# Kernel tuning notes

Hardware: AMD Instinct MI355X
Metric: run time of the kernel (lower is better)

Reference implementation:

```python
import jax, jax.numpy as jnp
import numpy as np

N = 16384      # nodes
E = 262144     # edges (avg degree 16)
H = 128        # hidden_channels
F = 128        # num_filters
G = 50         # num_gaussians
L = 6          # num_interactions
NG = 16        # graphs in batch
CUTOFF = 10.0
BOX = 5.0
LN2 = 0.6931471805599453


def _ssp(x):  # ShiftedSoftplus
    return jax.nn.softplus(x) - LN2


def setup_inputs() -> dict:
    key = jax.random.key(0)
    ks = jax.random.split(key, 20)
    w = lambda k, shape: jax.random.normal(k, shape, dtype=jnp.float32) * 0.1
    return {
        "z": jax.random.randint(ks[0], (N,), 0, 2),
        "pos": jax.random.uniform(ks[1], (N, 3), dtype=jnp.float32) * BOX,
        "edge_index": jax.random.randint(ks[2], (2, E), 0, N),
        "batch": jnp.sort(jax.random.randint(ks[3], (N,), 0, NG)),
        "emb": w(ks[4], (2, H)),
        "mlp_w1": w(ks[5], (L, G, F)),
        "mlp_b1": jnp.zeros((L, F), jnp.float32),
        "mlp_w2": w(ks[6], (L, F, F)),
        "mlp_b2": jnp.zeros((L, F), jnp.float32),
        "cf_w1": w(ks[7], (L, H, F)),
        "cf_w2": w(ks[8], (L, F, H)),
        "cf_b2": jnp.zeros((L, H), jnp.float32),
        "lin_w": w(ks[9], (L, H, H)),
        "lin_b": jnp.zeros((L, H), jnp.float32),
        "out_w1": w(ks[10], (H, H // 2)),
        "out_b1": jnp.zeros((H // 2,), jnp.float32),
        "out_w2": w(ks[11], (H // 2, 1)),
        "out_b2": jnp.zeros((1,), jnp.float32),
    }


def reference(z, pos, edge_index, batch, emb, mlp_w1, mlp_b1, mlp_w2, mlp_b2,
              cf_w1, cf_w2, cf_b2, lin_w, lin_b, out_w1, out_b1, out_w2, out_b2):
    row, col = edge_index[0], edge_index[1]  # message flows row -> col
    dx = pos[row] - pos[col]
    dx = dx - jnp.round(dx / BOX) * BOX      # minimum-image PBC
    ew = jnp.sqrt(jnp.sum(dx * dx, axis=-1))               # [E]
    offset = jnp.linspace(0.0, CUTOFF, G)
    coeff = -0.5 / (offset[1] - offset[0]) ** 2
    ea = jnp.exp(coeff * (ew[:, None] - offset[None, :]) ** 2)  # [E, G]
    C = 0.5 * (jnp.cos(ew * jnp.pi / CUTOFF) + 1.0)
    C = C * (ew < CUTOFF).astype(C.dtype)                   # [E]

    h = emb[z]                                              # [N, H]
    for l in range(L):
        # continuous filter from smeared distances, with cosine cutoff
        W = (_ssp(ea @ mlp_w1[l] + mlp_b1[l]) @ mlp_w2[l] + mlp_b2[l]) * C[:, None]  # [E, F]
        xh = h @ cf_w1[l]                                   # [N, F] (lin1, no bias)
        msg = xh[row] * W                                   # gather x_j, modulate
        agg = jax.ops.segment_sum(msg, col, num_segments=N)  # scatter-add
        xc = agg @ cf_w2[l] + cf_b2[l]                      # [N, H] (lin2)
        h = h + (_ssp(xc) @ lin_w[l] + lin_b[l])            # residual interaction

    h = _ssp(h @ out_w1 + out_b1) @ out_w2 + out_b2         # [N, 1]
    out = jax.ops.segment_sum(h, batch, num_segments=NG)    # readout 'add'
    return jax.nn.sigmoid(out)                              # [NG, 1]
```

## Files before the change

### kernel.cpp

```cpp
#include <hip/hip_runtime.h>
#include <math.h>

#define N_NODES 16384
#define N_EDGES 262144
#define HDIM    128
#define NG50    50
#define NLAYER  6
#define NGRAPH  16
#define TROWS   1025
#define RMAXF   4.34f
#define WPL     16384

__device__ __forceinline__ float ssp_f(float x){
  return (x > 20.0f ? x : log1pf(__expf(x))) - 0.6931471805599453f;
}
__device__ __forceinline__ void fma4(float4& c, float a, const float4 b){
  c.x = fmaf(a,b.x,c.x); c.y = fmaf(a,b.y,c.y); c.z = fmaf(a,b.z,c.z); c.w = fmaf(a,b.w,c.w);
}
__device__ __forceinline__ unsigned short f2bf(float x){
  unsigned u = __float_as_uint(x);
  u += 0x7FFF + ((u>>16)&1);
  return (unsigned short)(u>>16);
}
__device__ __forceinline__ float bf2f(unsigned short u){
  return __uint_as_float(((unsigned)u)<<16);
}
__device__ __forceinline__ void load_chunk(float* Bs, const float* W, int kc, int tid){
  const float4* src = (const float4*)(W + kc*HDIM);
  float4* dst = (float4*)Bs;
  #pragma unroll
  for (int i=0;i<4;++i) dst[tid + i*256] = src[tid + i*256];
}

typedef __attribute__((ext_vector_type(8))) short bf16x8;
typedef __attribute__((ext_vector_type(4))) float f32x4;
__device__ __forceinline__ int swzf(int lin){ return lin ^ (((lin>>9)&7)<<4); }

__device__ __forceinline__ void split8(const float4 v0, const float4 v1, bf16x8& hi, bf16x8& lo){
  float x[8] = {v0.x,v0.y,v0.z,v0.w,v1.x,v1.y,v1.z,v1.w};
  #pragma unroll
  for (int i=0;i<8;++i){
    unsigned short h = f2bf(x[i]);
    hi[i] = (short)h;
    lo[i] = (short)f2bf(x[i] - bf2f(h));
  }
}

__global__ __launch_bounds__(256) void k_init_h(const int* __restrict__ z,
    const float* __restrict__ emb, float* __restrict__ h){
  int t = blockIdx.x*256 + threadIdx.x;
  int n = t >> 5, q = t & 31;
  ((float4*)h)[t] = ((const float4*)emb)[(z[n]<<5) + q];
}

#define TAB_R  4
#define TAB_NB 257
__global__ __launch_bounds__(256) void k_tab(const float* __restrict__ w1, const float* __restrict__ b1,
      const float* __restrict__ w2, const float* __restrict__ b2, float* __restrict__ tab){
  __shared__ float ea[TAB_R][52];
  __shared__ float sT[TAB_R][HDIM];
  __shared__ float part[2][TAB_R][HDIM];
  int l  = blockIdx.x / TAB_NB;
  int i0 = (blockIdx.x % TAB_NB) * TAB_R;
  int tid = threadIdx.x;
  int j    = tid & 127;
  int half = tid >> 7;
  const float* w1l = w1 + (size_t)l*NG50*HDIM;
  const float* w2l = w2 + (size_t)l*HDIM*HDIM;
  float* tabl = tab + (size_t)l*TROWS*HDIM;
  const float STEP = RMAXF/1024.0f;
  const float GS   = 10.0f/49.0f;
  const float GC   = -0.5f/(GS*GS);
  if (tid < TAB_R*NG50){
    int rr = tid / NG50, k = tid - rr*NG50;
    int ri = i0 + rr; if (ri > TROWS-1) ri = TROWS-1;
    float d = ri*STEP - k*GS;
    ea[rr][k] = __expf(GC*d*d);
  }
  __syncthreads();
  {
    float acc[TAB_R] = {0,0,0,0};
    int kb = half*25;
    for (int k=0;k<25;++k){
      float wv = w1l[(kb+k)*HDIM + j];
      #pragma unroll
      for (int r=0;r<TAB_R;++r) acc[r] = fmaf(ea[r][kb+k], wv, acc[r]);
    }
    #pragma unroll
    for (int r=0;r<TAB_R;++r) part[half][r][j] = acc[r];
  }
  __syncthreads();
  {
    float b1v = b1[(size_t)l*HDIM + j];
    #pragma unroll
    for (int rr=0;rr<2;++rr){
      int r = half*2 + rr;
      sT[r][j] = ssp_f(part[0][r][j] + part[1][r][j] + b1v);
    }
  }
  __syncthreads();
  {
    float o[TAB_R] = {0,0,0,0};
    int kb = half*64;
    #pragma unroll 4
    for (int k=0;k<64;++k){
      float wv = w2l[(kb+k)*HDIM + j];
      #pragma unroll
      for (int r=0;r<TAB_R;++r) o[r] = fmaf(sT[r][kb+k], wv, o[r]);
    }
    #pragma unroll
    for (int r=0;r<TAB_R;++r) part[half][r][j] = o[r];
  }
  __syncthreads();
  {
    float b2v = b2[(size_t)l*HDIM + j];
    #pragma unroll
    for (int rr=0;rr<2;++rr){
      int r = half*2 + rr;
      int ri = i0 + r;
      if (ri < TROWS){
        float rv = ri*STEP;
        float C = 0.5f*(cosf(rv*0.31415926535897931f) + 1.0f);
        tabl[(size_t)ri*HDIM + j] = (part[0][r][j] + part[1][r][j] + b2v)*C;
      }
    }
  }
}

__global__ __launch_bounds__(256) void k_pack(const float* __restrict__ tab, ushort4* __restrict__ tabp){
  size_t t = (size_t)blockIdx.x*256 + threadIdx.x;
  int lane = (int)(t & 63);
  size_t row = t >> 6;
  size_t l = row >> 10, i = row & 1023;
  const float* a = tab + (l*TROWS + i)*HDIM + lane*2;
  float2 av = *(const float2*)a;
  float2 bv = *(const float2*)(a + HDIM);
  ushort4 p;
  p.x = f2bf(av.x); p.y = f2bf(av.y); p.z = f2bf(bv.x); p.w = f2bf(bv.y);
  tabp[t] = p;
}

__global__ __launch_bounds__(256) void k_wpack(const float* __restrict__ cf_w2,
    const float* __restrict__ lin_w, const float* __restrict__ cf_w1, ushort* __restrict__ wp){
  int b   = blockIdx.x;
  int mat = b >> 3;
  int s   = (b & 7)*256 + threadIdx.x;
  const float* M = (mat < 6)  ? cf_w2 + (size_t)mat*HDIM*HDIM
                 : (mat < 12) ? lin_w + (size_t)(mat-6)*HDIM*HDIM
                              : cf_w1 + (size_t)(mat-12)*HDIM*HDIM;
  int ct = s >> 8, ks = (s >> 6) & 3, l = s & 63;
  int col = ct*16 + (l & 15);
  int r0  = ks*32 + (l >> 4)*8;
  ushort oh[8], ol[8];
  #pragma unroll
  for (int i=0;i<8;++i){
    float w = M[(size_t)(r0+i)*HDIM + col];
    oh[i] = f2bf(w);
    ol[i] = f2bf(w - bf2f(oh[i]));
  }
  ushort* dh = wp + (size_t)(2*mat)*WPL + (size_t)s*8;
  ushort* dl = dh + WPL;
  *(ushort4*)(dh+0) = make_ushort4(oh[0],oh[1],oh[2],oh[3]);
  *(ushort4*)(dh+4) = make_ushort4(oh[4],oh[5],oh[6],oh[7]);
  *(ushort4*)(dl+0) = make_ushort4(ol[0],ol[1],ol[2],ol[3]);
  *(ushort4*)(dl+4) = make_ushort4(ol[4],ol[5],ol[6],ol[7]);
}

__global__ __launch_bounds__(256) void k_hist(const int* __restrict__ ei, int* __restrict__ cursor){
  int e = blockIdx.x*256 + threadIdx.x;
  if (e < N_EDGES) atomicAdd(&cursor[ei[N_EDGES + e]], 1);
}
__global__ __launch_bounds__(1024) void k_scan(int* __restrict__ cursor, int* __restrict__ rowptr){
  __shared__ int sbuf[1024];
  int t = threadIdx.x;
  int base = t*16;
  int d[16]; int s = 0;
  #pragma unroll
  for (int i=0;i<16;++i){ d[i] = cursor[base+i]; s += d[i]; }
  sbuf[t] = s; __syncthreads();
  for (int off=1; off<1024; off<<=1){
    int v = sbuf[t];
    int add = (t >= off) ? sbuf[t-off] : 0;
    __syncthreads();
    sbuf[t] = v + add;
    __syncthreads();
  }
  int run = (t==0) ? 0 : sbuf[t-1];
  #pragma unroll
  for (int i=0;i<16;++i){ rowptr[base+i] = run; cursor[base+i] = run; run += d[i]; }
  if (t==1023) rowptr[N_NODES] = run;
}
__global__ __launch_bounds__(256) void k_fill(const int* __restrict__ ei, const float* __restrict__ pos,
    int* __restrict__ cursor, int* __restrict__ srcl, float* __restrict__ tl){
  int e = blockIdx.x*256 + threadIdx.x;
  if (e < N_EDGES){
    int a = ei[e];
    int c = ei[N_EDGES + e];
    float dx = pos[3*a+0] - pos[3*c+0];
    float dy = pos[3*a+1] - pos[3*c+1];
    float dz = pos[3*a+2] - pos[3*c+2];
    dx -= rintf(dx*0.2f)*5.0f;
    dy -= rintf(dy*0.2f)*5.0f;
    dz -= rintf(dz*0.2f)*5.0f;
    float r = sqrtf(fmaf(dx,dx,fmaf(dy,dy,dz*dz)));
    int slot = atomicAdd(&cursor[c], 1);
    srcl[slot] = a;
    tl[slot]   = r * (1024.0f/RMAXF);
  }
}

#define FR 16
__global__ __launch_bounds__(256,4) void k_gemm_xh(const float* __restrict__ A,
    const float* __restrict__ B, ushort4* __restrict__ Cb){
  __shared__ float Bs[32*HDIM];
  int tid = threadIdx.x;
  int m0 = blockIdx.x*FR;
  int tc = tid & 31, tr = tid >> 5;
  int j0 = tc*4;
  int lr0 = tr*2, lr1 = tr*2+1;
  float4 acc0 = make_float4(0,0,0,0), acc1 = acc0;
  const float* A0 = A + (size_t)(m0 + lr0)*HDIM;
  const float* A1 = A + (size_t)(m0 + lr1)*HDIM;
  for (int kc=0; kc<HDIM; kc+=32){
    __syncthreads();
    load_chunk(Bs, B, kc, tid);
    __syncthreads();
    #pragma unroll
    for (int kk=0; kk<32; kk+=4){
      float4 b0 = *(const float4*)(Bs + (kk+0)*HDIM + j0);
      float4 b1 = *(const float4*)(Bs + (kk+1)*HDIM + j0);
      float4 b2 = *(const float4*)(Bs + (kk+2)*HDIM + j0);
      float4 b3 = *(const float4*)(Bs + (kk+3)*HDIM + j0);
      float4 a0 = *(const float4*)(A0 + kc + kk);
      float4 a1 = *(const float4*)(A1 + kc + kk);
      fma4(acc0,a0.x,b0); fma4(acc0,a0.y,b1); fma4(acc0,a0.z,b2); fma4(acc0,a0.w,b3);
      fma4(acc1,a1.x,b0); fma4(acc1,a1.y,b1); fma4(acc1,a1.z,b2); fma4(acc1,a1.w,b3);
    }
  }
  ushort4 o;
  o.x=f2bf(acc0.x); o.y=f2bf(acc0.y); o.z=f2bf(acc0.z); o.w=f2bf(acc0.w);
  Cb[(size_t)(m0 + lr0)*32 + tc] = o;
  o.x=f2bf(acc1.x); o.y=f2bf(acc1.y); o.z=f2bf(acc1.z); o.w=f2bf(acc1.w);
  Cb[(size_t)(m0 + lr1)*32 + tc] = o;
}

__global__ __launch_bounds__(256) void k_agg(const int* __restrict__ rowptr,
    const int* __restrict__ srcl, const float* __restrict__ tl,
    const ushort4* __restrict__ tabp, const ushort2* __restrict__ xhb, float* __restrict__ agg){
  int c = blockIdx.x*4 + (threadIdx.x >> 6);
  int lane = threadIdx.x & 63;
  int beg = rowptr[c], end = rowptr[c+1];
  const ushort4* tabl = tabp + lane;
  const ushort2* xh2  = xhb + lane;
  float ax = 0.f, ay = 0.f;
  for (int k0 = beg; k0 < end; k0 += 64){
    int rem = end - k0;
    int cnt = rem < 64 ? rem : 64;
    int   s_l = 0; float t_l = 0.f;
    if (lane < cnt){ s_l = srcl[k0+lane]; t_l = tl[k0+lane]; }
    int j = 0;
    for (; j+3 < cnt; j += 4){
      int   r0 = __shfl(s_l, j,   64);
      float t0 = __shfl(t_l, j,   64);
      int   r1 = __shfl(s_l, j+1, 64);
      float t1 = __shfl(t_l, j+1, 64);
      int   r2 = __shfl(s_l, j+2, 64);
      float t2 = __shfl(t_l, j+2, 64);
      int   r3 = __shfl(s_l, j+3, 64);
      float t3 = __shfl(t_l, j+3, 64);
      int i00 = (int)t0; if (i00 > 1023) i00 = 1023;
      int i01 = (int)t1; if (i01 > 1023) i01 = 1023;
      int i02 = (int)t2; if (i02 > 1023) i02 = 1023;
      int i03 = (int)t3; if (i03 > 1023) i03 = 1023;
      float f0 = t0 - (float)i00;
      float f1 = t1 - (float)i01;
      float f2 = t2 - (float)i02;
      float f3 = t3 - (float)i03;
      ushort4 p0 = tabl[(size_t)i00*64];
      ushort4 p1 = tabl[(size_t)i01*64];
      ushort4 p2 = tabl[(size_t)i02*64];
      ushort4 p3 = tabl[(size_t)i03*64];
      ushort2 x0 = xh2[(size_t)r0*64];
      ushort2 x1 = xh2[(size_t)r1*64];
      ushort2 x2 = xh2[(size_t)r2*64];
      ushort2 x3 = xh2[(size_t)r3*64];
      float a0x=bf2f(p0.x), a0y=bf2f(p0.y), d0x=bf2f(p0.z)-a0x, d0y=bf2f(p0.w)-a0y;
      float a1x=bf2f(p1.x), a1y=bf2f(p1.y), d1x=bf2f(p1.z)-a1x, d1y=bf2f(p1.w)-a1y;
      float a2x=bf2f(p2.x), a2y=bf2f(p2.y), d2x=bf2f(p2.z)-a2x, d2y=bf2f(p2.w)-a2y;
      float a3x=bf2f(p3.x), a3y=bf2f(p3.y), d3x=bf2f(p3.z)-a3x, d3y=bf2f(p3.w)-a3y;
      ax = fmaf(bf2f(x0.x), fmaf(f0, d0x, a0x), ax);
      ay = fmaf(bf2f(x0.y), fmaf(f0, d0y, a0y), ay);
      ax = fmaf(bf2f(x1.x), fmaf(f1, d1x, a1x), ax);
      ay = fmaf(bf2f(x1.y), fmaf(f1, d1y, a1y), ay);
      ax = fmaf(bf2f(x2.x), fmaf(f2, d2x, a2x), ax);
      ay = fmaf(bf2f(x2.y), fmaf(f2, d2y, a2y), ay);
      ax = fmaf(bf2f(x3.x), fmaf(f3, d3x, a3x), ax);
      ay = fmaf(bf2f(x3.y), fmaf(f3, d3y, a3y), ay);
    }
    for (; j < cnt; ++j){
      int   r0 = __shfl(s_l, j, 64);
      float t0 = __shfl(t_l, j, 64);
      int i00 = (int)t0; if (i00 > 1023) i00 = 1023;
      float f0 = t0 - (float)i00;
      ushort4 p0 = tabl[(size_t)i00*64];
      ushort2 x0 = xh2[(size_t)r0*64];
      float a0x=bf2f(p0.x), a0y=bf2f(p0.y), d0x=bf2f(p0.z)-a0x, d0y=bf2f(p0.w)-a0y;
      ax = fmaf(bf2f(x0.x), fmaf(f0, d0x, a0x), ax);
      ay = fmaf(bf2f(x0.y), fmaf(f0, d0y, a0y), ay);
    }
  }
  ((float2*)(agg + (size_t)c*HDIM))[lane] = make_float2(ax, ay);
}

__device__ __forceinline__ void gemm_hl(const ushort* plane, size_t wfo,
    const bf16x8* ah, const bf16x8* al, f32x4* acc){
  #pragma unroll
  for (int ks=0;ks<4;++ks){
    #pragma unroll
    for (int c=0;c<2;++c){
      const ushort* p = plane + wfo + (size_t)(c*4+ks)*512;
      bf16x8 wh = *(const bf16x8*)p;
      bf16x8 wl = *(const bf16x8*)(p + WPL);
      acc[c] = __builtin_amdgcn_mfma_f32_16x16x32_bf16(ah[ks], wh, acc[c], 0,0,0);
      acc[c] = __builtin_amdgcn_mfma_f32_16x16x32_bf16(al[ks], wh, acc[c], 0,0,0);
      acc[c] = __builtin_amdgcn_mfma_f32_16x16x32_bf16(ah[ks], wl, acc[c], 0,0,0);
    }
  }
}
template<bool LAST>
__global__ __launch_bounds__(256,4) void k_fused_mfma(
    const float* __restrict__ agg,
    const ushort* __restrict__ w2p, const float* __restrict__ B2,
    const ushort* __restrict__ wlp, const float* __restrict__ BL,
    float* __restrict__ Hio,
    const ushort* __restrict__ w1p, ushort* __restrict__ Xout)
{
  __shared__ alignas(16) float S[16*HDIM];
  const int tid = threadIdx.x;
  const int wv  = tid >> 6, l = tid & 63;
  const int m   = l & 15, g = l >> 4;
  const int m0  = blockIdx.x * 16;
  const int colA = wv*32 + m;
  const int colB = colA + 16;
  const size_t wfo = (size_t)(wv*8*64 + l)*8;

  const f32x4 vzero = {0.f,0.f,0.f,0.f};
  bf16x8 ah[4], al[4];
  f32x4 acc[2];

  #pragma unroll
  for (int ks=0;ks<4;++ks){
    const float* p = agg + (size_t)(m0+m)*HDIM + ks*32 + g*8;
    split8(*(const float4*)p, *(const float4*)(p+4), ah[ks], al[ks]);
  }
  acc[0] = vzero; acc[1] = vzero;
  gemm_hl(w2p, wfo, ah, al, acc);
  {
    const float b20 = B2[colA], b21 = B2[colB];
    #pragma unroll
    for (int r=0;r<4;++r){
      const int row = g*4 + r;
      *(float*)((char*)S + swzf(row*512 + colA*4)) = ssp_f(acc[0][r] + b20);
      *(float*)((char*)S + swzf(row*512 + colB*4)) = ssp_f(acc[1][r] + b21);
    }
  }
  __syncthreads();

  #pragma unroll
  for (int ks=0;ks<4;++ks){
    int lin = m*512 + (ks*32 + g*8)*4;
    split8(*(const float4*)((const char*)S + swzf(lin)),
           *(const float4*)((const char*)S + swzf(lin + 16)), ah[ks], al[ks]);
  }
  float hr0[4], hr1[4];
  #pragma unroll
  for (int r=0;r<4;++r){
    hr0[r] = Hio[(size_t)(m0 + g*4 + r)*HDIM + colA];
    hr1[r] = Hio[(size_t)(m0 + g*4 + r)*HDIM + colB];
  }
  acc[0] = vzero; acc[1] = vzero;
  gemm_hl(wlp, wfo, ah, al, acc);
  __syncthreads();
  {
    const float bl0 = BL[colA], bl1 = BL[colB];
    #pragma unroll
    for (int r=0;r<4;++r){
      const int row = g*4 + r;
      float v0 = hr0[r] + acc[0][r] + bl0;
      float v1 = hr1[r] + acc[1][r] + bl1;
      Hio[(size_t)(m0+row)*HDIM + colA] = v0;
      Hio[(size_t)(m0+row)*HDIM + colB] = v1;
      if (!LAST){
        *(float*)((char*)S + swzf(row*512 + colA*4)) = v0;
        *(float*)((char*)S + swzf(row*512 + colB*4)) = v1;
      }
    }
  }
  if (LAST) return;
  __syncthreads();

  #pragma unroll
  for (int ks=0;ks<4;++ks){
    int lin = m*512 + (ks*32 + g*8)*4;
    split8(*(const float4*)((const char*)S + swzf(lin)),
           *(const float4*)((const char*)S + swzf(lin + 16)), ah[ks], al[ks]);
  }
  acc[0] = vzero; acc[1] = vzero;
  gemm_hl(w1p, wfo, ah, al, acc);
  #pragma unroll
  for (int r=0;r<4;++r){
    const int row = g*4 + r;
    Xout[(size_t)(m0+row)*HDIM + colA] = f2bf(acc[0][r]);
    Xout[(size_t)(m0+row)*HDIM + colB] = f2bf(acc[1][r]);
  }
}

__global__ __launch_bounds__(256) void k_outA(const float* __restrict__ h, const float* __restrict__ w1,
    const float* __restrict__ b1, const float* __restrict__ w2, const float* __restrict__ b2,
    float* __restrict__ nodeval){
  int node = blockIdx.x*4 + (threadIdx.x >> 6);
  int lane = threadIdx.x & 63;
  float acc = b1[lane];
  const float* hrow = h + (size_t)node*HDIM;
  #pragma unroll 4
  for (int k=0;k<HDIM;++k) acc = fmaf(hrow[k], w1[k*64 + lane], acc);
  float s = ssp_f(acc) * w2[lane];
  for (int off=32; off>0; off>>=1) s += __shfl_down(s, off, 64);
  if (lane == 0) nodeval[node] = s + b2[0];
}

__global__ __launch_bounds__(256) void k_outB(const float* __restrict__ nodeval,
    const int* __restrict__ batch, float* __restrict__ out){
  __shared__ float sred[4];
  int g = blockIdx.x;
  int t = threadIdx.x;
  float s = 0.f;
  for (int n = t; n < N_NODES; n += 256)
    if (batch[n] == g) s += nodeval[n];
  for (int off=32; off>0; off>>=1) s += __shfl_down(s, off, 64);
  if ((t & 63) == 0) sred[t >> 6] = s;
  __syncthreads();
  if (t == 0){
    float tot = sred[0] + sred[1] + sred[2] + sred[3];
    out[g] = 1.0f/(1.0f + __expf(-tot));
  }
}

extern "C" void kernel_launch(void* const* d_in, const int* in_sizes, int n_in,
                              void* d_out, int out_size, void* d_ws, size_t ws_size,
                              hipStream_t stream){
  (void)in_sizes; (void)n_in; (void)out_size;
  const int*   z      = (const int*)  d_in[0];
  const float* pos    = (const float*)d_in[1];
  const int*   ei     = (const int*)  d_in[2];
  const int*   batch  = (const int*)  d_in[3];
  const float* emb    = (const float*)d_in[4];
  const float* mlp_w1 = (const float*)d_in[5];
  const float* mlp_b1 = (const float*)d_in[6];
  const float* mlp_w2 = (const float*)d_in[7];
  const float* mlp_b2 = (const float*)d_in[8];
  const float* cf_w1  = (const float*)d_in[9];
  const float* cf_w2  = (const float*)d_in[10];
  const float* cf_b2  = (const float*)d_in[11];
  const float* lin_w  = (const float*)d_in[12];
  const float* lin_b  = (const float*)d_in[13];
  const float* ow1    = (const float*)d_in[14];
  const float* ob1    = (const float*)d_in[15];
  const float* ow2    = (const float*)d_in[16];
  const float* ob2    = (const float*)d_in[17];

  char* wp = (char*)d_ws;
  size_t used = 0;
  auto alloc = [&](size_t bytes)->char*{
    char* p = wp + used;
    used += (bytes + 1023) & ~(size_t)1023;
    return p;
  };
  float*   tab     = (float*)alloc((size_t)NLAYER*TROWS*HDIM*4);
  ushort4* tabp    = (ushort4*)alloc((size_t)NLAYER*1024*64*8);
  float*   h       = (float*)alloc((size_t)N_NODES*HDIM*4);
  ushort4* xhb     = (ushort4*)alloc((size_t)N_NODES*32*8);
  float*   agg     = (float*)alloc((size_t)N_NODES*HDIM*4);
  ushort*  wpk     = (ushort*)alloc((size_t)36*WPL*2);
  int*     rowptr  = (int*)  alloc((size_t)(N_NODES+1)*4);
  int*     cursor  = (int*)  alloc((size_t)N_NODES*4);
  int*     srcl    = (int*)  alloc((size_t)N_EDGES*4);
  float*   tl      = (float*)alloc((size_t)N_EDGES*4);
  float*   nodeval = (float*)alloc((size_t)N_NODES*4);
  if (used > ws_size) return;

  hipMemsetAsync(cursor, 0, (size_t)N_NODES*4, stream);

  k_init_h<<<N_NODES*32/256, 256, 0, stream>>>(z, emb, h);
  k_tab   <<<NLAYER*TAB_NB, 256, 0, stream>>>(mlp_w1, mlp_b1, mlp_w2, mlp_b2, tab);
  k_pack  <<<NLAYER*1024*64/256, 256, 0, stream>>>(tab, tabp);
  k_wpack <<<144, 256, 0, stream>>>(cf_w2, lin_w, cf_w1, wpk);
  k_hist  <<<N_EDGES/256, 256, 0, stream>>>(ei, cursor);
  k_scan  <<<1, 1024, 0, stream>>>(cursor, rowptr);
  k_fill  <<<N_EDGES/256, 256, 0, stream>>>(ei, pos, cursor, srcl, tl);

  k_gemm_xh<<<N_NODES/FR, 256, 0, stream>>>(h, cf_w1, xhb);
  for (int l=0; l<NLAYER; ++l){
    k_agg<<<N_NODES/4, 256, 0, stream>>>(rowptr, srcl, tl,
                 tabp + (size_t)l*1024*64, (const ushort2*)xhb, agg);
    const ushort* w2p = wpk + (size_t)(2*l)*WPL;
    const ushort* wlp = wpk + (size_t)(2*(6+l))*WPL;
    if (l < NLAYER-1){
      const ushort* w1p = wpk + (size_t)(2*(13+l))*WPL;
      k_fused_mfma<false><<<N_NODES/16, 256, 0, stream>>>(agg,
                 w2p, cf_b2 + (size_t)l*HDIM, wlp, lin_b + (size_t)l*HDIM, h,
                 w1p, (ushort*)xhb);
    } else {
      k_fused_mfma<true><<<N_NODES/16, 256, 0, stream>>>(agg,
                 w2p, cf_b2 + (size_t)l*HDIM, wlp, lin_b + (size_t)l*HDIM, h,
                 nullptr, nullptr);
    }
  }
  k_outA  <<<N_NODES/4, 256, 0, stream>>>(h, ow1, ob1, ow2, ob2, nodeval);
  k_outB  <<<NGRAPH, 256, 0, stream>>>(nodeval, batch, (float*)d_out);
}
```

Before: 433.6 us.

## Fuse edge aggregation into per-layer MFMA kernel and merge setup kernels

```diff
diff --git a/kernel.cpp b/kernel.cpp
--- a/kernel.cpp
+++ b/kernel.cpp
@@ -25,12 +25,6 @@
 __device__ __forceinline__ float bf2f(unsigned short u){
   return __uint_as_float(((unsigned)u)<<16);
 }
-__device__ __forceinline__ void load_chunk(float* Bs, const float* W, int kc, int tid){
-  const float4* src = (const float4*)(W + kc*HDIM);
-  float4* dst = (float4*)Bs;
-  #pragma unroll
-  for (int i=0;i<4;++i) dst[tid + i*256] = src[tid + i*256];
-}
 
 typedef __attribute__((ext_vector_type(8))) short bf16x8;
 typedef __attribute__((ext_vector_type(4))) float f32x4;
@@ -46,175 +40,195 @@
   }
 }
 
-__global__ __launch_bounds__(256) void k_init_h(const int* __restrict__ z,
-    const float* __restrict__ emb, float* __restrict__ h){
-  int t = blockIdx.x*256 + threadIdx.x;
-  int n = t >> 5, q = t & 31;
-  ((float4*)h)[t] = ((const float4*)emb)[(z[n]<<5) + q];
-}
-
-#define TAB_R  4
-#define TAB_NB 257
-__global__ __launch_bounds__(256) void k_tab(const float* __restrict__ w1, const float* __restrict__ b1,
-      const float* __restrict__ w2, const float* __restrict__ b2, float* __restrict__ tab){
+#define TAB_R   4
+#define TAB_NB  257
+#define B_INIT  2048
+#define B_TAB   1542
+#define B_HIST  1024
+#define B_WPACK 144
+#define K1_GRID (B_INIT + B_TAB + B_HIST + B_WPACK)
+
+__global__ __launch_bounds__(256) void k_setup1(
+    const int* __restrict__ z, const float* __restrict__ emb, float* __restrict__ h,
+    const float* __restrict__ w1, const float* __restrict__ b1,
+    const float* __restrict__ w2, const float* __restrict__ b2, float* __restrict__ tab,
+    const int* __restrict__ ei, int* __restrict__ cursor,
+    const float* __restrict__ cf_w2, const float* __restrict__ lin_w,
+    const float* __restrict__ cf_w1, ushort* __restrict__ wp)
+{
   __shared__ float ea[TAB_R][52];
   __shared__ float sT[TAB_R][HDIM];
   __shared__ float part[2][TAB_R][HDIM];
-  int l  = blockIdx.x / TAB_NB;
-  int i0 = (blockIdx.x % TAB_NB) * TAB_R;
-  int tid = threadIdx.x;
-  int j    = tid & 127;
-  int half = tid >> 7;
-  const float* w1l = w1 + (size_t)l*NG50*HDIM;
-  const float* w2l = w2 + (size_t)l*HDIM*HDIM;
-  float* tabl = tab + (size_t)l*TROWS*HDIM;
-  const float STEP = RMAXF/1024.0f;
-  const float GS   = 10.0f/49.0f;
-  const float GC   = -0.5f/(GS*GS);
-  if (tid < TAB_R*NG50){
-    int rr = tid / NG50, k = tid - rr*NG50;
-    int ri = i0 + rr; if (ri > TROWS-1) ri = TROWS-1;
-    float d = ri*STEP - k*GS;
-    ea[rr][k] = __expf(GC*d*d);
-  }
-  __syncthreads();
+  const int b = blockIdx.x;
+  const int tid = threadIdx.x;
+
+  if (b < B_INIT){
+    int t = b*256 + tid;
+    int n = t >> 5, q = t & 31;
+    ((float4*)h)[t] = ((const float4*)emb)[(z[n]<<5) + q];
+    return;
+  }
+  if (b < B_INIT + B_TAB){
+    int bb = b - B_INIT;
+    int l  = bb / TAB_NB;
+    int i0 = (bb % TAB_NB) * TAB_R;
+    int j    = tid & 127;
+    int half = tid >> 7;
+    const float* w1l = w1 + (size_t)l*NG50*HDIM;
+    const float* w2l = w2 + (size_t)l*HDIM*HDIM;
+    float* tabl = tab + (size_t)l*TROWS*HDIM;
+    const float STEP = RMAXF/1024.0f;
+    const float GS   = 10.0f/49.0f;
+    const float GC   = -0.5f/(GS*GS);
+    if (tid < TAB_R*NG50){
+      int rr = tid / NG50, k = tid - rr*NG50;
+      int ri = i0 + rr; if (ri > TROWS-1) ri = TROWS-1;
+      float d = ri*STEP - k*GS;
+      ea[rr][k] = __expf(GC*d*d);
+    }
+    __syncthreads();
+    {
+      float acc[TAB_R] = {0,0,0,0};
+      int kb = half*25;
+      for (int k=0;k<25;++k){
+        float wv = w1l[(kb+k)*HDIM + j];
+        #pragma unroll
+        for (int r=0;r<TAB_R;++r) acc[r] = fmaf(ea[r][kb+k], wv, acc[r]);
+      }
+      #pragma unroll
+      for (int r=0;r<TAB_R;++r) part[half][r][j] = acc[r];
+    }
+    __syncthreads();
+    {
+      float b1v = b1[(size_t)l*HDIM + j];
+      #pragma unroll
+      for (int rr=0;rr<2;++rr){
+        int r = half*2 + rr;
+        sT[r][j] = ssp_f(part[0][r][j] + part[1][r][j] + b1v);
+      }
+    }
+    __syncthreads();
+    {
+      float o[TAB_R] = {0,0,0,0};
+      int kb = half*64;
+      #pragma unroll 4
+      for (int k=0;k<64;++k){
+        float wv = w2l[(kb+k)*HDIM + j];
+        #pragma unroll
+        for (int r=0;r<TAB_R;++r) o[r] = fmaf(sT[r][kb+k], wv, o[r]);
+      }
+      #pragma unroll
+      for (int r=0;r<TAB_R;++r) part[half][r][j] = o[r];
+    }
+    __syncthreads();
+    {
+      float b2v = b2[(size_t)l*HDIM + j];
+      #pragma unroll
+      for (int rr=0;rr<2;++rr){
+        int r = half*2 + rr;
+        int ri = i0 + r;
+        if (ri < TROWS){
+          float rv = ri*STEP;
+          float C = 0.5f*(cosf(rv*0.31415926535897931f) + 1.0f);
+          tabl[(size_t)ri*HDIM + j] = (part[0][r][j] + part[1][r][j] + b2v)*C;
+        }
+      }
+    }
+    return;
+  }
+  if (b < B_INIT + B_TAB + B_HIST){
+    int e = (b - (B_INIT + B_TAB))*256 + tid;
+    if (e < N_EDGES) atomicAdd(&cursor[ei[N_EDGES + e]], 1);
+    return;
+  }
   {
-    float acc[TAB_R] = {0,0,0,0};
-    int kb = half*25;
-    for (int k=0;k<25;++k){
-      float wv = w1l[(kb+k)*HDIM + j];
-      #pragma unroll
-      for (int r=0;r<TAB_R;++r) acc[r] = fmaf(ea[r][kb+k], wv, acc[r]);
-    }
-    #pragma unroll
-    for (int r=0;r<TAB_R;++r) part[half][r][j] = acc[r];
-  }
-  __syncthreads();
-  {
-    float b1v = b1[(size_t)l*HDIM + j];
-    #pragma unroll
-    for (int rr=0;rr<2;++rr){
-      int r = half*2 + rr;
-      sT[r][j] = ssp_f(part[0][r][j] + part[1][r][j] + b1v);
-    }
-  }
-  __syncthreads();
-  {
-    float o[TAB_R] = {0,0,0,0};
-    int kb = half*64;
-    #pragma unroll 4
-    for (int k=0;k<64;++k){
-      float wv = w2l[(kb+k)*HDIM + j];
-      #pragma unroll
-      for (int r=0;r<TAB_R;++r) o[r] = fmaf(sT[r][kb+k], wv, o[r]);
-    }
-    #pragma unroll
-    for (int r=0;r<TAB_R;++r) part[half][r][j] = o[r];
-  }
-  __syncthreads();
-  {
-    float b2v = b2[(size_t)l*HDIM + j];
-    #pragma unroll
-    for (int rr=0;rr<2;++rr){
-      int r = half*2 + rr;
-      int ri = i0 + r;
-      if (ri < TROWS){
-        float rv = ri*STEP;
-        float C = 0.5f*(cosf(rv*0.31415926535897931f) + 1.0f);
-        tabl[(size_t)ri*HDIM + j] = (part[0][r][j] + part[1][r][j] + b2v)*C;
-      }
-    }
-  }
-}
-
-__global__ __launch_bounds__(256) void k_pack(const float* __restrict__ tab, ushort4* __restrict__ tabp){
-  size_t t = (size_t)blockIdx.x*256 + threadIdx.x;
-  int lane = (int)(t & 63);
-  size_t row = t >> 6;
+    int bb  = b - (B_INIT + B_TAB + B_HIST);
+    int mat = bb >> 3;
+    int s   = (bb & 7)*256 + tid;
+    const float* M = (mat < 6)  ? cf_w2 + (size_t)mat*HDIM*HDIM
+                   : (mat < 12) ? lin_w + (size_t)(mat-6)*HDIM*HDIM
+                                : cf_w1 + (size_t)(mat-12)*HDIM*HDIM;
+    int ct = s >> 8, ks = (s >> 6) & 3, l = s & 63;
+    int col = ct*16 + (l & 15);
+    int r0  = ks*32 + (l >> 4)*8;
+    ushort oh[8], ol[8];
+    #pragma unroll
+    for (int i=0;i<8;++i){
+      float w = M[(size_t)(r0+i)*HDIM + col];
+      oh[i] = f2bf(w);
+      ol[i] = f2bf(w - bf2f(oh[i]));
+    }
+    ushort* dh = wp + (size_t)(2*mat)*WPL + (size_t)s*8;
+    ushort* dl = dh + WPL;
+    *(ushort4*)(dh+0) = make_ushort4(oh[0],oh[1],oh[2],oh[3]);
+    *(ushort4*)(dh+4) = make_ushort4(oh[4],oh[5],oh[6],oh[7]);
+    *(ushort4*)(dl+0) = make_ushort4(ol[0],ol[1],ol[2],ol[3]);
+    *(ushort4*)(dl+4) = make_ushort4(ol[4],ol[5],ol[6],ol[7]);
+  }
+}
+
+__global__ __launch_bounds__(1024) void k_scan_pack(int* __restrict__ cursor,
+    int* __restrict__ rowptr, const float* __restrict__ tab, ushort4* __restrict__ tabp){
+  __shared__ int sbuf[1024];
+  int t = threadIdx.x;
+  if (blockIdx.x == 0){
+    int base = t*16;
+    int d[16]; int s = 0;
+    #pragma unroll
+    for (int i=0;i<16;++i){ d[i] = cursor[base+i]; s += d[i]; }
+    sbuf[t] = s; __syncthreads();
+    for (int off=1; off<1024; off<<=1){
+      int v = sbuf[t];
+      int add = (t >= off) ? sbuf[t-off] : 0;
+      __syncthreads();
+      sbuf[t] = v + add;
+      __syncthreads();
+    }
+    int run = (t==0) ? 0 : sbuf[t-1];
+    #pragma unroll
+    for (int i=0;i<16;++i){ rowptr[base+i] = run; cursor[base+i] = run; run += d[i]; }
+    if (t==1023) rowptr[N_NODES] = run;
+    return;
+  }
+  size_t tt = (size_t)(blockIdx.x-1)*1024 + t;
+  int lane = (int)(tt & 63);
+  size_t row = tt >> 6;
   size_t l = row >> 10, i = row & 1023;
   const float* a = tab + (l*TROWS + i)*HDIM + lane*2;
   float2 av = *(const float2*)a;
   float2 bv = *(const float2*)(a + HDIM);
   ushort4 p;
   p.x = f2bf(av.x); p.y = f2bf(av.y); p.z = f2bf(bv.x); p.w = f2bf(bv.y);
-  tabp[t] = p;
-}
-
-__global__ __launch_bounds__(256) void k_wpack(const float* __restrict__ cf_w2,
-    const float* __restrict__ lin_w, const float* __restrict__ cf_w1, ushort* __restrict__ wp){
-  int b   = blockIdx.x;
-  int mat = b >> 3;
-  int s   = (b & 7)*256 + threadIdx.x;
-  const float* M = (mat < 6)  ? cf_w2 + (size_t)mat*HDIM*HDIM
-                 : (mat < 12) ? lin_w + (size_t)(mat-6)*HDIM*HDIM
-                              : cf_w1 + (size_t)(mat-12)*HDIM*HDIM;
-  int ct = s >> 8, ks = (s >> 6) & 3, l = s & 63;
-  int col = ct*16 + (l & 15);
-  int r0  = ks*32 + (l >> 4)*8;
-  ushort oh[8], ol[8];
-  #pragma unroll
-  for (int i=0;i<8;++i){
-    float w = M[(size_t)(r0+i)*HDIM + col];
-    oh[i] = f2bf(w);
-    ol[i] = f2bf(w - bf2f(oh[i]));
-  }
-  ushort* dh = wp + (size_t)(2*mat)*WPL + (size_t)s*8;
-  ushort* dl = dh + WPL;
-  *(ushort4*)(dh+0) = make_ushort4(oh[0],oh[1],oh[2],oh[3]);
-  *(ushort4*)(dh+4) = make_ushort4(oh[4],oh[5],oh[6],oh[7]);
-  *(ushort4*)(dl+0) = make_ushort4(ol[0],ol[1],ol[2],ol[3]);
-  *(ushort4*)(dl+4) = make_ushort4(ol[4],ol[5],ol[6],ol[7]);
-}
-
-__global__ __launch_bounds__(256) void k_hist(const int* __restrict__ ei, int* __restrict__ cursor){
-  int e = blockIdx.x*256 + threadIdx.x;
-  if (e < N_EDGES) atomicAdd(&cursor[ei[N_EDGES + e]], 1);
-}
-__global__ __launch_bounds__(1024) void k_scan(int* __restrict__ cursor, int* __restrict__ rowptr){
-  __shared__ int sbuf[1024];
-  int t = threadIdx.x;
-  int base = t*16;
-  int d[16]; int s = 0;
-  #pragma unroll
-  for (int i=0;i<16;++i){ d[i] = cursor[base+i]; s += d[i]; }
-  sbuf[t] = s; __syncthreads();
-  for (int off=1; off<1024; off<<=1){
-    int v = sbuf[t];
-    int add = (t >= off) ? sbuf[t-off] : 0;
-    __syncthreads();
-    sbuf[t] = v + add;
-    __syncthreads();
-  }
-  int run = (t==0) ? 0 : sbuf[t-1];
-  #pragma unroll
-  for (int i=0;i<16;++i){ rowptr[base+i] = run; cursor[base+i] = run; run += d[i]; }
-  if (t==1023) rowptr[N_NODES] = run;
-}
-__global__ __launch_bounds__(256) void k_fill(const int* __restrict__ ei, const float* __restrict__ pos,
-    int* __restrict__ cursor, int* __restrict__ srcl, float* __restrict__ tl){
-  int e = blockIdx.x*256 + threadIdx.x;
-  if (e < N_EDGES){
-    int a = ei[e];
-    int c = ei[N_EDGES + e];
-    float dx = pos[3*a+0] - pos[3*c+0];
-    float dy = pos[3*a+1] - pos[3*c+1];
-    float dz = pos[3*a+2] - pos[3*c+2];
-    dx -= rintf(dx*0.2f)*5.0f;
-    dy -= rintf(dy*0.2f)*5.0f;
-    dz -= rintf(dz*0.2f)*5.0f;
-    float r = sqrtf(fmaf(dx,dx,fmaf(dy,dy,dz*dz)));
-    int slot = atomicAdd(&cursor[c], 1);
-    srcl[slot] = a;
-    tl[slot]   = r * (1024.0f/RMAXF);
-  }
+  tabp[tt] = p;
 }
 
 #define FR 16
-__global__ __launch_bounds__(256,4) void k_gemm_xh(const float* __restrict__ A,
-    const float* __restrict__ B, ushort4* __restrict__ Cb){
+__global__ __launch_bounds__(256,4) void k_fill_xh(
+    const int* __restrict__ ei, const float* __restrict__ pos,
+    int* __restrict__ cursor, int* __restrict__ srcl, float* __restrict__ tl,
+    const float* __restrict__ A, const float* __restrict__ B, ushort4* __restrict__ Cb)
+{
   __shared__ float Bs[32*HDIM];
-  int tid = threadIdx.x;
-  int m0 = blockIdx.x*FR;
+  const int tid = threadIdx.x;
+  if (blockIdx.x < 1024){
+    int e = blockIdx.x*256 + tid;
+    if (e < N_EDGES){
+      int a = ei[e];
+      int c = ei[N_EDGES + e];
+      float dx = pos[3*a+0] - pos[3*c+0];
+      float dy = pos[3*a+1] - pos[3*c+1];
+      float dz = pos[3*a+2] - pos[3*c+2];
+      dx -= rintf(dx*0.2f)*5.0f;
+      dy -= rintf(dy*0.2f)*5.0f;
+      dz -= rintf(dz*0.2f)*5.0f;
+      float r = sqrtf(fmaf(dx,dx,fmaf(dy,dy,dz*dz)));
+      int slot = atomicAdd(&cursor[c], 1);
+      srcl[slot] = a;
+      tl[slot]   = r * (1024.0f/RMAXF);
+    }
+    return;
+  }
+  int m0 = (blockIdx.x - 1024)*FR;
   int tc = tid & 31, tr = tid >> 5;
   int j0 = tc*4;
   int lr0 = tr*2, lr1 = tr*2+1;
@@ -223,7 +237,12 @@
   const float* A1 = A + (size_t)(m0 + lr1)*HDIM;
   for (int kc=0; kc<HDIM; kc+=32){
     __syncthreads();
-    load_chunk(Bs, B, kc, tid);
+    {
+      const float4* src = (const float4*)(B + kc*HDIM);
+      float4* dst = (float4*)Bs;
+      #pragma unroll
+      for (int i=0;i<4;++i) dst[tid + i*256] = src[tid + i*256];
+    }
     __syncthreads();
     #pragma unroll
     for (int kk=0; kk<32; kk+=4){
@@ -244,74 +263,6 @@
   Cb[(size_t)(m0 + lr1)*32 + tc] = o;
 }
 
-__global__ __launch_bounds__(256) void k_agg(const int* __restrict__ rowptr,
-    const int* __restrict__ srcl, const float* __restrict__ tl,
-    const ushort4* __restrict__ tabp, const ushort2* __restrict__ xhb, float* __restrict__ agg){
-  int c = blockIdx.x*4 + (threadIdx.x >> 6);
-  int lane = threadIdx.x & 63;
-  int beg = rowptr[c], end = rowptr[c+1];
-  const ushort4* tabl = tabp + lane;
-  const ushort2* xh2  = xhb + lane;
-  float ax = 0.f, ay = 0.f;
-  for (int k0 = beg; k0 < end; k0 += 64){
-    int rem = end - k0;
-    int cnt = rem < 64 ? rem : 64;
-    int   s_l = 0; float t_l = 0.f;
-    if (lane < cnt){ s_l = srcl[k0+lane]; t_l = tl[k0+lane]; }
-    int j = 0;
-    for (; j+3 < cnt; j += 4){
-      int   r0 = __shfl(s_l, j,   64);
-      float t0 = __shfl(t_l, j,   64);
-      int   r1 = __shfl(s_l, j+1, 64);
-      float t1 = __shfl(t_l, j+1, 64);
-      int   r2 = __shfl(s_l, j+2, 64);
-      float t2 = __shfl(t_l, j+2, 64);
-      int   r3 = __shfl(s_l, j+3, 64);
-      float t3 = __shfl(t_l, j+3, 64);
-      int i00 = (int)t0; if (i00 > 1023) i00 = 1023;
-      int i01 = (int)t1; if (i01 > 1023) i01 = 1023;
-      int i02 = (int)t2; if (i02 > 1023) i02 = 1023;
-      int i03 = (int)t3; if (i03 > 1023) i03 = 1023;
-      float f0 = t0 - (float)i00;
-      float f1 = t1 - (float)i01;
-      float f2 = t2 - (float)i02;
-      float f3 = t3 - (float)i03;
-      ushort4 p0 = tabl[(size_t)i00*64];
-      ushort4 p1 = tabl[(size_t)i01*64];
-      ushort4 p2 = tabl[(size_t)i02*64];
-      ushort4 p3 = tabl[(size_t)i03*64];
-      ushort2 x0 = xh2[(size_t)r0*64];
-      ushort2 x1 = xh2[(size_t)r1*64];
-      ushort2 x2 = xh2[(size_t)r2*64];
-      ushort2 x3 = xh2[(size_t)r3*64];
-      float a0x=bf2f(p0.x), a0y=bf2f(p0.y), d0x=bf2f(p0.z)-a0x, d0y=bf2f(p0.w)-a0y;
-      float a1x=bf2f(p1.x), a1y=bf2f(p1.y), d1x=bf2f(p1.z)-a1x, d1y=bf2f(p1.w)-a1y;
-      float a2x=bf2f(p2.x), a2y=bf2f(p2.y), d2x=bf2f(p2.z)-a2x, d2y=bf2f(p2.w)-a2y;
-      float a3x=bf2f(p3.x), a3y=bf2f(p3.y), d3x=bf2f(p3.z)-a3x, d3y=bf2f(p3.w)-a3y;
-      ax = fmaf(bf2f(x0.x), fmaf(f0, d0x, a0x), ax);
-      ay = fmaf(bf2f(x0.y), fmaf(f0, d0y, a0y), ay);
-      ax = fmaf(bf2f(x1.x), fmaf(f1, d1x, a1x), ax);
-      ay = fmaf(bf2f(x1.y), fmaf(f1, d1y, a1y), ay);
-      ax = fmaf(bf2f(x2.x), fmaf(f2, d2x, a2x), ax);
-      ay = fmaf(bf2f(x2.y), fmaf(f2, d2y, a2y), ay);
-      ax = fmaf(bf2f(x3.x), fmaf(f3, d3x, a3x), ax);
-      ay = fmaf(bf2f(x3.y), fmaf(f3, d3y, a3y), ay);
-    }
-    for (; j < cnt; ++j){
-      int   r0 = __shfl(s_l, j, 64);
-      float t0 = __shfl(t_l, j, 64);
-      int i00 = (int)t0; if (i00 > 1023) i00 = 1023;
-      float f0 = t0 - (float)i00;
-      ushort4 p0 = tabl[(size_t)i00*64];
-      ushort2 x0 = xh2[(size_t)r0*64];
-      float a0x=bf2f(p0.x), a0y=bf2f(p0.y), d0x=bf2f(p0.z)-a0x, d0y=bf2f(p0.w)-a0y;
-      ax = fmaf(bf2f(x0.x), fmaf(f0, d0x, a0x), ax);
-      ay = fmaf(bf2f(x0.y), fmaf(f0, d0y, a0y), ay);
-    }
-  }
-  ((float2*)(agg + (size_t)c*HDIM))[lane] = make_float2(ax, ay);
-}
-
 __device__ __forceinline__ void gemm_hl(const ushort* plane, size_t wfo,
     const bf16x8* ah, const bf16x8* al, f32x4* acc){
   #pragma unroll
@@ -328,30 +279,100 @@
   }
 }
 template<bool LAST>
-__global__ __launch_bounds__(256,4) void k_fused_mfma(
-    const float* __restrict__ agg,
+__global__ __launch_bounds__(256,4) void k_layer(
+    const int* __restrict__ rowptr, const int* __restrict__ srcl, const float* __restrict__ tl,
+    const ushort4* __restrict__ tabp, const ushort2* __restrict__ xh_cur,
     const ushort* __restrict__ w2p, const float* __restrict__ B2,
     const ushort* __restrict__ wlp, const float* __restrict__ BL,
-    float* __restrict__ Hio,
-    const ushort* __restrict__ w1p, ushort* __restrict__ Xout)
+    float* __restrict__ Hio, const ushort* __restrict__ w1p, ushort* __restrict__ xh_nxt)
 {
-  __shared__ alignas(16) float S[16*HDIM];
-  const int tid = threadIdx.x;
-  const int wv  = tid >> 6, l = tid & 63;
-  const int m   = l & 15, g = l >> 4;
-  const int m0  = blockIdx.x * 16;
+  __shared__ alignas(16) float Sa[16*HDIM];
+  __shared__ alignas(16) float St[16*HDIM];
+  const int tid  = threadIdx.x;
+  const int wv   = tid >> 6, lane = tid & 63;
+  const int m0   = blockIdx.x * 16;
+
+  {
+    const ushort4* tabl = tabp + lane;
+    const ushort2* xh2  = xh_cur + lane;
+    for (int i=0;i<4;++i){
+      int c = m0 + wv*4 + i;
+      int beg = rowptr[c], end = rowptr[c+1];
+      float ax = 0.f, ay = 0.f;
+      for (int k0 = beg; k0 < end; k0 += 64){
+        int rem = end - k0;
+        int cnt = rem < 64 ? rem : 64;
+        int   s_l = 0; float t_l = 0.f;
+        if (lane < cnt){ s_l = srcl[k0+lane]; t_l = tl[k0+lane]; }
+        int j = 0;
+        for (; j+3 < cnt; j += 4){
+          int   r0 = __shfl(s_l, j,   64);
+          float t0 = __shfl(t_l, j,   64);
+          int   r1 = __shfl(s_l, j+1, 64);
+          float t1 = __shfl(t_l, j+1, 64);
+          int   r2 = __shfl(s_l, j+2, 64);
+          float t2 = __shfl(t_l, j+2, 64);
+          int   r3 = __shfl(s_l, j+3, 64);
+          float t3 = __shfl(t_l, j+3, 64);
+          int i00 = (int)t0; if (i00 > 1023) i00 = 1023;
+          int i01 = (int)t1; if (i01 > 1023) i01 = 1023;
+          int i02 = (int)t2; if (i02 > 1023) i02 = 1023;
+          int i03 = (int)t3; if (i03 > 1023) i03 = 1023;
+          float f0 = t0 - (float)i00;
+          float f1 = t1 - (float)i01;
+          float f2 = t2 - (float)i02;
+          float f3 = t3 - (float)i03;
+          ushort4 p0 = tabl[(size_t)i00*64];
+          ushort4 p1 = tabl[(size_t)i01*64];
+          ushort4 p2 = tabl[(size_t)i02*64];
+          ushort4 p3 = tabl[(size_t)i03*64];
+          ushort2 x0 = xh2[(size_t)r0*64];
+          ushort2 x1 = xh2[(size_t)r1*64];
+          ushort2 x2 = xh2[(size_t)r2*64];
+          ushort2 x3 = xh2[(size_t)r3*64];
+          float a0x=bf2f(p0.x), a0y=bf2f(p0.y), d0x=bf2f(p0.z)-a0x, d0y=bf2f(p0.w)-a0y;
+          float a1x=bf2f(p1.x), a1y=bf2f(p1.y), d1x=bf2f(p1.z)-a1x, d1y=bf2f(p1.w)-a1y;
+          float a2x=bf2f(p2.x), a2y=bf2f(p2.y), d2x=bf2f(p2.z)-a2x, d2y=bf2f(p2.w)-a2y;
+          float a3x=bf2f(p3.x), a3y=bf2f(p3.y), d3x=bf2f(p3.z)-a3x, d3y=bf2f(p3.w)-a3y;
+          ax = fmaf(bf2f(x0.x), fmaf(f0, d0x, a0x), ax);
+          ay = fmaf(bf2f(x0.y), fmaf(f0, d0y, a0y), ay);
+          ax = fmaf(bf2f(x1.x), fmaf(f1, d1x, a1x), ax);
+          ay = fmaf(bf2f(x1.y), fmaf(f1, d1y, a1y), ay);
+          ax = fmaf(bf2f(x2.x), fmaf(f2, d2x, a2x), ax);
+          ay = fmaf(bf2f(x2.y), fmaf(f2, d2y, a2y), ay);
+          ax = fmaf(bf2f(x3.x), fmaf(f3, d3x, a3x), ax);
+          ay = fmaf(bf2f(x3.y), fmaf(f3, d3y, a3y), ay);
+        }
+        for (; j < cnt; ++j){
+          int   r0 = __shfl(s_l, j, 64);
+          float t0 = __shfl(t_l, j, 64);
+          int i00 = (int)t0; if (i00 > 1023) i00 = 1023;
+          float f0 = t0 - (float)i00;
+          ushort4 p0 = tabl[(size_t)i00*64];
+          ushort2 x0 = xh2[(size_t)r0*64];
+          float a0x=bf2f(p0.x), a0y=bf2f(p0.y), d0x=bf2f(p0.z)-a0x, d0y=bf2f(p0.w)-a0y;
+          ax = fmaf(bf2f(x0.x), fmaf(f0, d0x, a0x), ax);
+          ay = fmaf(bf2f(x0.y), fmaf(f0, d0y, a0y), ay);
+        }
+      }
+      *(float2*)((char*)Sa + swzf((wv*4+i)*512 + lane*8)) = make_float2(ax, ay);
+    }
+  }
+  __syncthreads();
+
+  const int m = lane & 15, g = lane >> 4;
   const int colA = wv*32 + m;
   const int colB = colA + 16;
-  const size_t wfo = (size_t)(wv*8*64 + l)*8;
-
+  const size_t wfo = (size_t)(wv*8*64 + lane)*8;
   const f32x4 vzero = {0.f,0.f,0.f,0.f};
   bf16x8 ah[4], al[4];
   f32x4 acc[2];
 
   #pragma unroll
   for (int ks=0;ks<4;++ks){
-    const float* p = agg + (size_t)(m0+m)*HDIM + ks*32 + g*8;
-    split8(*(const float4*)p, *(const float4*)(p+4), ah[ks], al[ks]);
+    int lin = m*512 + (ks*32 + g*8)*4;
+    split8(*(const float4*)((const char*)Sa + swzf(lin)),
+           *(const float4*)((const char*)Sa + swzf(lin + 16)), ah[ks], al[ks]);
   }
   acc[0] = vzero; acc[1] = vzero;
   gemm_hl(w2p, wfo, ah, al, acc);
@@ -360,8 +381,8 @@
     #pragma unroll
     for (int r=0;r<4;++r){
       const int row = g*4 + r;
-      *(float*)((char*)S + swzf(row*512 + colA*4)) = ssp_f(acc[0][r] + b20);
-      *(float*)((char*)S + swzf(row*512 + colB*4)) = ssp_f(acc[1][r] + b21);
+      *(float*)((char*)St + swzf(row*512 + colA*4)) = ssp_f(acc[0][r] + b20);
+      *(float*)((char*)St + swzf(row*512 + colB*4)) = ssp_f(acc[1][r] + b21);
     }
   }
   __syncthreads();
@@ -369,8 +390,8 @@
   #pragma unroll
   for (int ks=0;ks<4;++ks){
     int lin = m*512 + (ks*32 + g*8)*4;
-    split8(*(const float4*)((const char*)S + swzf(lin)),
-           *(const float4*)((const char*)S + swzf(lin + 16)), ah[ks], al[ks]);
+    split8(*(const float4*)((const char*)St + swzf(lin)),
+           *(const float4*)((const char*)St + swzf(lin + 16)), ah[ks], al[ks]);
   }
   float hr0[4], hr1[4];
   #pragma unroll
@@ -380,7 +401,6 @@
   }
   acc[0] = vzero; acc[1] = vzero;
   gemm_hl(wlp, wfo, ah, al, acc);
-  __syncthreads();
   {
     const float bl0 = BL[colA], bl1 = BL[colB];
     #pragma unroll
@@ -391,8 +411,8 @@
       Hio[(size_t)(m0+row)*HDIM + colA] = v0;
       Hio[(size_t)(m0+row)*HDIM + colB] = v1;
       if (!LAST){
-        *(float*)((char*)S + swzf(row*512 + colA*4)) = v0;
-        *(float*)((char*)S + swzf(row*512 + colB*4)) = v1;
+        *(float*)((char*)Sa + swzf(row*512 + colA*4)) = v0;
+        *(float*)((char*)Sa + swzf(row*512 + colB*4)) = v1;
       }
     }
   }
@@ -402,16 +422,16 @@
   #pragma unroll
   for (int ks=0;ks<4;++ks){
     int lin = m*512 + (ks*32 + g*8)*4;
-    split8(*(const float4*)((const char*)S + swzf(lin)),
-           *(const float4*)((const char*)S + swzf(lin + 16)), ah[ks], al[ks]);
+    split8(*(const float4*)((const char*)Sa + swzf(lin)),
+           *(const float4*)((const char*)Sa + swzf(lin + 16)), ah[ks], al[ks]);
   }
   acc[0] = vzero; acc[1] = vzero;
   gemm_hl(w1p, wfo, ah, al, acc);
   #pragma unroll
   for (int r=0;r<4;++r){
     const int row = g*4 + r;
-    Xout[(size_t)(m0+row)*HDIM + colA] = f2bf(acc[0][r]);
-    Xout[(size_t)(m0+row)*HDIM + colB] = f2bf(acc[1][r]);
+    xh_nxt[(size_t)(m0+row)*HDIM + colA] = f2bf(acc[0][r]);
+    xh_nxt[(size_t)(m0+row)*HDIM + colB] = f2bf(acc[1][r]);
   }
 }
 
@@ -479,8 +499,8 @@
   float*   tab     = (float*)alloc((size_t)NLAYER*TROWS*HDIM*4);
   ushort4* tabp    = (ushort4*)alloc((size_t)NLAYER*1024*64*8);
   float*   h       = (float*)alloc((size_t)N_NODES*HDIM*4);
-  ushort4* xhb     = (ushort4*)alloc((size_t)N_NODES*32*8);
-  float*   agg     = (float*)alloc((size_t)N_NODES*HDIM*4);
+  ushort*  xhb0    = (ushort*)alloc((size_t)N_NODES*HDIM*2);
+  ushort*  xhb1    = (ushort*)alloc((size_t)N_NODES*HDIM*2);
   ushort*  wpk     = (ushort*)alloc((size_t)36*WPL*2);
   int*     rowptr  = (int*)  alloc((size_t)(N_NODES+1)*4);
   int*     cursor  = (int*)  alloc((size_t)N_NODES*4);
@@ -491,27 +511,25 @@
 
   hipMemsetAsync(cursor, 0, (size_t)N_NODES*4, stream);
 
-  k_init_h<<<N_NODES*32/256, 256, 0, stream>>>(z, emb, h);
-  k_tab   <<<NLAYER*TAB_NB, 256, 0, stream>>>(mlp_w1, mlp_b1, mlp_w2, mlp_b2, tab);
-  k_pack  <<<NLAYER*1024*64/256, 256, 0, stream>>>(tab, tabp);
-  k_wpack <<<144, 256, 0, stream>>>(cf_w2, lin_w, cf_w1, wpk);
-  k_hist  <<<N_EDGES/256, 256, 0, stream>>>(ei, cursor);
-  k_scan  <<<1, 1024, 0, stream>>>(cursor, rowptr);
-  k_fill  <<<N_EDGES/256, 256, 0, stream>>>(ei, pos, cursor, srcl, tl);
-
-  k_gemm_xh<<<N_NODES/FR, 256, 0, stream>>>(h, cf_w1, xhb);
+  k_setup1<<<K1_GRID, 256, 0, stream>>>(z, emb, h,
+      mlp_w1, mlp_b1, mlp_w2, mlp_b2, tab, ei, cursor, cf_w2, lin_w, cf_w1, wpk);
+  k_scan_pack<<<385, 1024, 0, stream>>>(cursor, rowptr, tab, tabp);
+  k_fill_xh<<<2048, 256, 0, stream>>>(ei, pos, cursor, srcl, tl, h, cf_w1, (ushort4*)xhb0);
+
   for (int l=0; l<NLAYER; ++l){
-    k_agg<<<N_NODES/4, 256, 0, stream>>>(rowptr, srcl, tl,
-                 tabp + (size_t)l*1024*64, (const ushort2*)xhb, agg);
     const ushort* w2p = wpk + (size_t)(2*l)*WPL;
     const ushort* wlp = wpk + (size_t)(2*(6+l))*WPL;
+    const ushort2* xcur = (const ushort2*)((l & 1) ? xhb1 : xhb0);
+    ushort*        xnxt = (l & 1) ? xhb0 : xhb1;
     if (l < NLAYER-1){
       const ushort* w1p = wpk + (size_t)(2*(13+l))*WPL;
-      k_fused_mfma<false><<<N_NODES/16, 256, 0, stream>>>(agg,
+      k_layer<false><<<N_NODES/16, 256, 0, stream>>>(rowptr, srcl, tl,
+                 tabp + (size_t)l*1024*64, xcur,
                  w2p, cf_b2 + (size_t)l*HDIM, wlp, lin_b + (size_t)l*HDIM, h,
-                 w1p, (ushort*)xhb);
+                 w1p, xnxt);
     } else {
-      k_fused_mfma<true><<<N_NODES/16, 256, 0, stream>>>(agg,
+      k_layer<true><<<N_NODES/16, 256, 0, stream>>>(rowptr, srcl, tl,
+                 tabp + (size_t)l*1024*64, xcur,
                  w2p, cf_b2 + (size_t)l*HDIM, wlp, lin_b + (size_t)l*HDIM, h,
                  nullptr, nullptr);
     }
```

New measurement: 395.6 us. -8.8%, faster.
